# Kernel optimization log

Hardware: AMD Instinct MI355X
Metric: run time of the kernel (lower is better)

Reference implementation:

```python
import jax, jax.numpy as jnp
import numpy as np

N = 50000          # nodes
E = 1000000        # edges (avg degree 20)
F_IN = 16          # fluidFeatures
LAYERS = [64, 64, 64, 2]
TERMS = 4          # basisTerms
DIM = 2            # spatial dim
EDGE_DIM = TERMS * DIM  # mode='cat' -> terms * dim = 8
OUT_SCALE = 1.0 / 128.0  # outputScaling


def fourier_basis(n_terms, x):
    """Fourier basis ('ffourier'): k=0 -> 1, odd k -> sin(pi*ceil(k/2)*x), even k -> cos(pi*(k/2)*x). x: [E] -> [E, n_terms]."""
    cols = []
    for k in range(n_terms):
        if k == 0:
            cols.append(jnp.ones_like(x))
        elif k % 2 == 1:
            cols.append(jnp.sin(jnp.pi * ((k + 1) // 2) * x))
        else:
            cols.append(jnp.cos(jnp.pi * (k // 2) * x))
    return jnp.stack(cols, axis=-1)


def edge_basis(edge_lengths):
    # basisEncoderLayer with mode='cat': per-component basis, concatenated -> [E, TERMS*DIM]
    return jnp.concatenate([fourier_basis(TERMS, edge_lengths[:, d]) for d in range(DIM)], axis=1)


def setup_inputs() -> dict:
    key = jax.random.key(0)
    k_x, k_ei, k_el, k_w = jax.random.split(key, 4)
    x = jax.random.normal(k_x, (N, F_IN), dtype=jnp.float32)
    edge_index = jax.random.randint(k_ei, (2, E), 0, N)
    edge_lengths = jax.random.uniform(k_el, (E, DIM), dtype=jnp.float32, minval=-1.0, maxval=1.0)
    # continuous-conv weights: [EDGE_DIM, in_feat, out_feat] per layer (uniform-style init)
    weights = {}
    in_f = F_IN
    wkeys = jax.random.split(k_w, len(LAYERS))
    for i, out_f in enumerate(LAYERS):
        scale = 1.0 / np.sqrt(EDGE_DIM * in_f)
        weights[f"W{i}"] = scale * jax.random.normal(wkeys[i], (EDGE_DIM, in_f, out_f), dtype=jnp.float32)
        in_f = out_f
    return dict(x=x, edge_index=edge_index, edge_lengths=edge_lengths, **weights)


def reference(x, edge_index, edge_lengths, W0, W1, W2, W3):
    src = edge_index[0]
    dst = edge_index[1]
    basis = edge_basis(edge_lengths)            # [E, EDGE_DIM]
    Ws = [W0, W1, W2, W3]
    h = x
    for i, W in enumerate(Ws):
        # gather sender features, contract with per-edge basis and conv weight, scatter-sum to receivers
        msg = jnp.einsum('eb,ef,bfo->eo', basis, h[src], W)   # [E, out]
        agg = jax.ops.segment_sum(msg, dst, num_segments=N)   # [N, out]
        h = jax.nn.relu(agg) if i < len(Ws) - 1 else agg
    return h * OUT_SCALE
```

## Files before the change

kernel.cpp:

```cpp
#include <hip/hip_runtime.h>
#include <hip/hip_bf16.h>
#include <math.h>

#define PI_F 3.14159265358979323846f
#define BK_SHIFT 8
#define P2_CHUNK 4096
#define P2_PER_THREAD 16

typedef __attribute__((ext_vector_type(8))) short bf16x8;
typedef __attribute__((ext_vector_type(4))) float f32x4;
typedef __attribute__((ext_vector_type(4))) unsigned short u16x4;
typedef __attribute__((ext_vector_type(8))) unsigned short u16x8;

__device__ __forceinline__ float bf2f(unsigned short u) {
    union { unsigned int i; float f; } v;
    v.i = ((unsigned int)u) << 16;
    return v.f;
}

__device__ __forceinline__ unsigned short f2bf_bits(float f) {
    __hip_bfloat16 b = __float2bfloat16(f);
    unsigned short u;
    __builtin_memcpy(&u, &b, 2);
    return u;
}


__global__ void count_kernel(const int* __restrict__ dst, int* __restrict__ cnt, int E) {
    int e = blockIdx.x * 256 + threadIdx.x;
    if (e < E) atomicAdd(&cnt[dst[e]], 1);
}

__global__ __launch_bounds__(256) void scan_reduce_kernel(const int* __restrict__ cnt,
                                                          int* __restrict__ bsum, int n) {
    __shared__ int sd[4];
    int idx = blockIdx.x * 256 + threadIdx.x;
    int v = (idx < n) ? cnt[idx] : 0;
    int s = v;
#pragma unroll
    for (int m = 1; m < 64; m <<= 1) s += __shfl_xor(s, m, 64);
    int wave = threadIdx.x >> 6;
    if ((threadIdx.x & 63) == 0) sd[wave] = s;
    __syncthreads();
    if (threadIdx.x == 0) bsum[blockIdx.x] = sd[0] + sd[1] + sd[2] + sd[3];
}

__global__ __launch_bounds__(256) void scan_top_kernel(const int* __restrict__ bsum,
                                                       int* __restrict__ boffs, int nb) {
    __shared__ int sd[256];
    int tid = threadIdx.x;
    int v = (tid < nb) ? bsum[tid] : 0;
    sd[tid] = v;
    __syncthreads();
#pragma unroll
    for (int off = 1; off < 256; off <<= 1) {
        int t = (tid >= off) ? sd[tid - off] : 0;
        __syncthreads();
        sd[tid] += t;
        __syncthreads();
    }
    if (tid < nb) boffs[tid] = sd[tid] - v;
}

__global__ __launch_bounds__(256) void scan_apply_kernel(int* __restrict__ cntcur,
                                                         int* __restrict__ offs,
                                                         const int* __restrict__ boffs,
                                                         int n, int total) {
    __shared__ int sd[256];
    int tid = threadIdx.x;
    int idx = blockIdx.x * 256 + tid;
    int v = (idx < n) ? cntcur[idx] : 0;
    sd[tid] = v;
    __syncthreads();
#pragma unroll
    for (int off = 1; off < 256; off <<= 1) {
        int t = (tid >= off) ? sd[tid - off] : 0;
        __syncthreads();
        sd[tid] += t;
        __syncthreads();
    }
    if (idx < n) offs[idx] = boffs[blockIdx.x] + sd[tid] - v;
    if (idx == 0) offs[n] = total;
}

__global__ void bucket_init_kernel(const int* __restrict__ offs, int* __restrict__ bucketCursor,
                                   int nbuk, int nN) {
    int b = blockIdx.x * 256 + threadIdx.x;
    if (b < nbuk) bucketCursor[b] = offs[min(b << BK_SHIFT, nN)];
}

__global__ __launch_bounds__(256) void bucket_scatter_kernel(const int* __restrict__ dst,
                                                             int* __restrict__ bucketCursor,
                                                             int* __restrict__ inter,
                                                             int E, int nbuk) {
    __shared__ int lcnt[256];
    __shared__ int lbase[256];
    __shared__ int lgpos[256];
    __shared__ int lsort[P2_CHUNK];
    __shared__ unsigned char lbuk[P2_CHUNK];
    int tid = threadIdx.x;
    int base = blockIdx.x * P2_CHUNK;
    lcnt[tid] = 0;
    __syncthreads();
    int myb[P2_PER_THREAD], myr[P2_PER_THREAD];
#pragma unroll
    for (int i = 0; i < P2_PER_THREAD; i++) {
        int idx = base + i * 256 + tid;
        int b = -1, r = 0;
        if (idx < E) {
            b = dst[idx] >> BK_SHIFT;
            r = atomicAdd(&lcnt[b], 1);
        }
        myb[i] = b;
        myr[i] = r;
    }
    __syncthreads();
    int v = lcnt[tid];
    lbase[tid] = v;
    __syncthreads();
    for (int off = 1; off < 256; off <<= 1) {
        int t = (tid >= off) ? lbase[tid - off] : 0;
        __syncthreads();
        lbase[tid] += t;
        __syncthreads();
    }
    int excl = lbase[tid] - v;
    if (tid < nbuk && v > 0) lgpos[tid] = atomicAdd(&bucketCursor[tid], v);
    __syncthreads();
    lbase[tid] = excl;
    __syncthreads();
#pragma unroll
    for (int i = 0; i < P2_PER_THREAD; i++) {
        if (myb[i] >= 0) {
            int p = lbase[myb[i]] + myr[i];
            lsort[p] = base + i * 256 + tid;
            lbuk[p] = (unsigned char)myb[i];
        }
    }
    __syncthreads();
    int total = (base + P2_CHUNK <= E) ? P2_CHUNK : (E > base ? E - base : 0);
    for (int idx = tid; idx < total; idx += 256) {
        int b = lbuk[idx];
        inter[lgpos[b] + (idx - lbase[b])] = lsort[idx];
    }
}

__global__ __launch_bounds__(256) void bucket_sort_fill_kernel(const int* __restrict__ inter,
                                                               const int* __restrict__ dst,
                                                               const int* __restrict__ src,
                                                               const float* __restrict__ el,
                                                               const int* __restrict__ offs,
                                                               int* __restrict__ srcS,
                                                               unsigned short* __restrict__ basisB,
                                                               int nN) {
    __shared__ int cursor[256];
    int b = blockIdx.x;
    int n0 = b << BK_SHIFT;
    int n1 = min(n0 + 256, nN);
    int tid = threadIdx.x;
    int p0 = offs[n0];
    int p1 = offs[n1];
    if (tid < n1 - n0) cursor[tid] = offs[n0 + tid];
    __syncthreads();
    for (int q = p0 + tid; q < p1; q += 256) {
        int e = inter[q];
        int d = dst[e];
        int pos = atomicAdd(&cursor[d - n0], 1);
        srcS[pos] = src[e];
        float2 xy = *(const float2*)(el + 2 * (size_t)e);
        u16x8 p;
        p[0] = f2bf_bits(1.0f);
        p[1] = f2bf_bits(__sinf(PI_F * xy.x));
        p[2] = f2bf_bits(__cosf(PI_F * xy.x));
        p[3] = f2bf_bits(__sinf(2.0f * PI_F * xy.x));
        p[4] = f2bf_bits(1.0f);
        p[5] = f2bf_bits(__sinf(PI_F * xy.y));
        p[6] = f2bf_bits(__cosf(PI_F * xy.y));
        p[7] = f2bf_bits(__sinf(2.0f * PI_F * xy.y));
        *(u16x8*)(basisB + (size_t)pos * 8) = p;
    }
}


__global__ void prep_w_kernel(const float* __restrict__ W, __hip_bfloat16* __restrict__ Wt, int K) {
    int i = blockIdx.x * 256 + threadIdx.x;
    if (i >= K * 64) return;
    int k = i >> 6, o = i & 63;
    Wt[(size_t)o * K + k] = __float2bfloat16(W[i]);
}

__global__ void prep_f2b_kernel(const float* __restrict__ in, __hip_bfloat16* __restrict__ out, int n) {
    int i = blockIdx.x * 256 + threadIdx.x;
    if (i < n) out[i] = __float2bfloat16(in[i]);
}


__device__ __forceinline__ void agg64_core(const unsigned short* __restrict__ hp,
                                           const int* __restrict__ srcS,
                                           const unsigned short* __restrict__ basisB,
                                           int start, int end, int eg, int fb,
                                           float acc[8][4]) {
    const int last = end - 1;
    int j = start;
    int qa = min(j + eg, last), qb = min(j + 4 + eg, last);
    int sa = srcS[qa], sb = srcS[qb];
    u16x4 ga = *(const u16x4*)(hp + (size_t)sa * 64 + fb);
    u16x4 gb = *(const u16x4*)(hp + (size_t)sb * 64 + fb);
    u16x8 ca = *(const u16x8*)(basisB + (size_t)qa * 8);
    u16x8 cb = *(const u16x8*)(basisB + (size_t)qb * 8);
    int qna = min(j + 8 + eg, last), qnb = min(j + 12 + eg, last);
    int sna = srcS[qna], snb = srcS[qnb];
    while (true) {
        int jn = j + 8;
        int q2a = min(jn + 8 + eg, last), q2b = min(jn + 12 + eg, last);
        int s2a = srcS[q2a], s2b = srcS[q2b];
        u16x4 gna = *(const u16x4*)(hp + (size_t)sna * 64 + fb);
        u16x4 gnb = *(const u16x4*)(hp + (size_t)snb * 64 + fb);
        u16x8 cna = *(const u16x8*)(basisB + (size_t)qna * 8);
        u16x8 cnb = *(const u16x8*)(basisB + (size_t)qnb * 8);
        float ha[4], hb[4];
        ha[0] = bf2f(ga[0]); ha[1] = bf2f(ga[1]); ha[2] = bf2f(ga[2]); ha[3] = bf2f(ga[3]);
        hb[0] = bf2f(gb[0]); hb[1] = bf2f(gb[1]); hb[2] = bf2f(gb[2]); hb[3] = bf2f(gb[3]);
        if (j + eg >= end)     { ha[0] = 0.f; ha[1] = 0.f; ha[2] = 0.f; ha[3] = 0.f; }
        if (j + 4 + eg >= end) { hb[0] = 0.f; hb[1] = 0.f; hb[2] = 0.f; hb[3] = 0.f; }
#pragma unroll
        for (int b = 0; b < 8; b++) {
            float w = bf2f(ca[b]);
#pragma unroll
            for (int c = 0; c < 4; c++) acc[b][c] += w * ha[c];
        }
#pragma unroll
        for (int b = 0; b < 8; b++) {
            float w = bf2f(cb[b]);
#pragma unroll
            for (int c = 0; c < 4; c++) acc[b][c] += w * hb[c];
        }
        if (jn >= end) break;
        j = jn;
        ga = gna; gb = gnb; ca = cna; cb = cnb;
        qna = q2a; qnb = q2b; sna = s2a; snb = s2b;
    }
}

__global__ __launch_bounds__(256) void agg64_kernel(const __hip_bfloat16* __restrict__ h,
                                                    const int* __restrict__ srcS,
                                                    const unsigned short* __restrict__ basisB,
                                                    const int* __restrict__ offs,
                                                    __hip_bfloat16* __restrict__ A, int nN) {
    int wid = (blockIdx.x * 256 + threadIdx.x) >> 6;
    int lane = threadIdx.x & 63;
    if (wid >= nN) return;
    int eg = lane >> 4, fg = lane & 15;
    int start = offs[wid], end = offs[wid + 1];
    float acc[8][4] = {};
    if (start < end)
        agg64_core((const unsigned short*)h, srcS, basisB, start, end, eg, fg * 4, acc);
#pragma unroll
    for (int b = 0; b < 8; b++) {
#pragma unroll
        for (int c = 0; c < 4; c++) {
            float v = acc[b][c];
            v += __shfl_xor(v, 16, 64);
            v += __shfl_xor(v, 32, 64);
            acc[b][c] = v;
        }
    }
    if (eg == 0) {
        unsigned short* Ar = (unsigned short*)A + (size_t)wid * 512;
#pragma unroll
        for (int b = 0; b < 8; b++) {
            u16x4 p;
            p[0] = f2bf_bits(acc[b][0]); p[1] = f2bf_bits(acc[b][1]);
            p[2] = f2bf_bits(acc[b][2]); p[3] = f2bf_bits(acc[b][3]);
            *(u16x4*)(Ar + b * 64 + fg * 4) = p;
        }
    }
}

__global__ __launch_bounds__(256) void agg_out_kernel(const __hip_bfloat16* __restrict__ h,
                                                      const int* __restrict__ srcS,
                                                      const unsigned short* __restrict__ basisB,
                                                      const int* __restrict__ offs,
                                                      const float* __restrict__ W3,
                                                      float* __restrict__ out, int nN) {
    int wid = (blockIdx.x * 256 + threadIdx.x) >> 6;
    int lane = threadIdx.x & 63;
    if (wid >= nN) return;
    int eg = lane >> 4, fg = lane & 15;
    int start = offs[wid], end = offs[wid + 1];
    float acc[8][4] = {};
    if (start < end)
        agg64_core((const unsigned short*)h, srcS, basisB, start, end, eg, fg * 4, acc);
#pragma unroll
    for (int b = 0; b < 8; b++) {
#pragma unroll
        for (int c = 0; c < 4; c++) {
            float v = acc[b][c];
            v += __shfl_xor(v, 16, 64);
            v += __shfl_xor(v, 32, 64);
            acc[b][c] = v;
        }
    }
    float o0 = 0.f, o1 = 0.f;
#pragma unroll
    for (int b = 0; b < 8; b++) {
        const float* w = W3 + (size_t)(b * 64 + fg * 4) * 2;
        float4 wa = *(const float4*)w;
        float4 wb = *(const float4*)(w + 4);
        o0 += acc[b][0] * wa.x + acc[b][1] * wa.z + acc[b][2] * wb.x + acc[b][3] * wb.z;
        o1 += acc[b][0] * wa.y + acc[b][1] * wa.w + acc[b][2] * wb.y + acc[b][3] * wb.w;
    }
#pragma unroll
    for (int m = 1; m < 16; m <<= 1) {
        o0 += __shfl_xor(o0, m, 64);
        o1 += __shfl_xor(o1, m, 64);
    }
    if (lane == 0) {
        out[(size_t)wid * 2 + 0] = o0 * (1.0f / 128.0f);
        out[(size_t)wid * 2 + 1] = o1 * (1.0f / 128.0f);
    }
}


__global__ __launch_bounds__(256) void agg16_kernel(const __hip_bfloat16* __restrict__ h,
                                                    const int* __restrict__ srcS,
                                                    const unsigned short* __restrict__ basisB,
                                                    const int* __restrict__ offs,
                                                    __hip_bfloat16* __restrict__ A, int nN) {
    int wid = (blockIdx.x * 256 + threadIdx.x) >> 6;
    int lane = threadIdx.x & 63;
    if (wid >= nN) return;
    int eg = lane >> 2, fg = lane & 3;
    int start = offs[wid], end = offs[wid + 1];
    float acc[8][4] = {};
    if (start < end) {
        const unsigned short* hp = (const unsigned short*)h;
        const int last = end - 1;
        const int fb = fg * 4;
        int j = start;
        int q = min(j + eg, last);
        int s = srcS[q];
        u16x4 g = *(const u16x4*)(hp + (size_t)s * 16 + fb);
        u16x8 cbv = *(const u16x8*)(basisB + (size_t)q * 8);
        int qn = min(j + 16 + eg, last);
        int sn = srcS[qn];
        while (true) {
            int jn = j + 16;
            int q2 = min(jn + 16 + eg, last);
            int s2 = srcS[q2];
            u16x4 gn = *(const u16x4*)(hp + (size_t)sn * 16 + fb);
            u16x8 cn = *(const u16x8*)(basisB + (size_t)qn * 8);
            float hv[4];
            hv[0] = bf2f(g[0]); hv[1] = bf2f(g[1]); hv[2] = bf2f(g[2]); hv[3] = bf2f(g[3]);
            if (j + eg >= end) { hv[0] = 0.f; hv[1] = 0.f; hv[2] = 0.f; hv[3] = 0.f; }
#pragma unroll
            for (int b = 0; b < 8; b++) {
                float w = bf2f(cbv[b]);
#pragma unroll
                for (int c = 0; c < 4; c++) acc[b][c] += w * hv[c];
            }
            if (jn >= end) break;
            j = jn;
            g = gn; cbv = cn; qn = q2; sn = s2;
        }
    }
#pragma unroll
    for (int b = 0; b < 8; b++) {
#pragma unroll
        for (int c = 0; c < 4; c++) {
            float v = acc[b][c];
            v += __shfl_xor(v, 4, 64);
            v += __shfl_xor(v, 8, 64);
            v += __shfl_xor(v, 16, 64);
            v += __shfl_xor(v, 32, 64);
            acc[b][c] = v;
        }
    }
    if (eg == 0) {
        unsigned short* Ar = (unsigned short*)A + (size_t)wid * 128;
#pragma unroll
        for (int b = 0; b < 8; b++) {
            u16x4 p;
            p[0] = f2bf_bits(acc[b][0]); p[1] = f2bf_bits(acc[b][1]);
            p[2] = f2bf_bits(acc[b][2]); p[3] = f2bf_bits(acc[b][3]);
            *(u16x4*)(Ar + b * 16 + fg * 4) = p;
        }
    }
}


template <int K, bool RELU>
__global__ __launch_bounds__(256) void gemm_mfma_kernel(const __hip_bfloat16* __restrict__ A,
                                                        const __hip_bfloat16* __restrict__ Wt,
                                                        __hip_bfloat16* __restrict__ Hout, int nN) {
    int wave = threadIdx.x >> 6;
    int lane = threadIdx.x & 63;
    int m16 = lane & 15;
    int kg = lane >> 4;
    int arow = blockIdx.x * 64 + wave * 16 + m16;
    bool rowok = arow < nN;
    const short* Ap = (const short*)A;
    const short* Wp = (const short*)Wt;
    size_t abase = (size_t)arow * K + kg * 8;
    size_t wb0 = (size_t)(0 * 16 + m16) * K + kg * 8;
    size_t wb1 = (size_t)(1 * 16 + m16) * K + kg * 8;
    size_t wb2 = (size_t)(2 * 16 + m16) * K + kg * 8;
    size_t wb3 = (size_t)(3 * 16 + m16) * K + kg * 8;
    f32x4 acc0 = {0.f, 0.f, 0.f, 0.f};
    f32x4 acc1 = {0.f, 0.f, 0.f, 0.f};
    f32x4 acc2 = {0.f, 0.f, 0.f, 0.f};
    f32x4 acc3 = {0.f, 0.f, 0.f, 0.f};
#pragma unroll 4
    for (int kc = 0; kc < K; kc += 32) {
        bf16x8 af = {};
        if (rowok) af = *(const bf16x8*)(Ap + abase + kc);
        bf16x8 b0 = *(const bf16x8*)(Wp + wb0 + kc);
        bf16x8 b1 = *(const bf16x8*)(Wp + wb1 + kc);
        bf16x8 b2 = *(const bf16x8*)(Wp + wb2 + kc);
        bf16x8 b3 = *(const bf16x8*)(Wp + wb3 + kc);
        acc0 = __builtin_amdgcn_mfma_f32_16x16x32_bf16(af, b0, acc0, 0, 0, 0);
        acc1 = __builtin_amdgcn_mfma_f32_16x16x32_bf16(af, b1, acc1, 0, 0, 0);
        acc2 = __builtin_amdgcn_mfma_f32_16x16x32_bf16(af, b2, acc2, 0, 0, 0);
        acc3 = __builtin_amdgcn_mfma_f32_16x16x32_bf16(af, b3, acc3, 0, 0, 0);
    }
    int orow0 = blockIdx.x * 64 + wave * 16 + kg * 4;
#pragma unroll
    for (int r = 0; r < 4; r++) {
        int row = orow0 + r;
        if (row < nN) {
            float v0 = acc0[r], v1 = acc1[r], v2 = acc2[r], v3 = acc3[r];
            if (RELU) {
                v0 = fmaxf(v0, 0.0f); v1 = fmaxf(v1, 0.0f);
                v2 = fmaxf(v2, 0.0f); v3 = fmaxf(v3, 0.0f);
            }
            __hip_bfloat16* Hr = Hout + (size_t)row * 64;
            Hr[0 * 16 + m16] = __float2bfloat16(v0);
            Hr[1 * 16 + m16] = __float2bfloat16(v1);
            Hr[2 * 16 + m16] = __float2bfloat16(v2);
            Hr[3 * 16 + m16] = __float2bfloat16(v3);
        }
    }
}


extern "C" void kernel_launch(void* const* d_in, const int* in_sizes, int n_in,
                              void* d_out, int out_size, void* d_ws, size_t ws_size,
                              hipStream_t stream) {
    const float* x  = (const float*)d_in[0];
    const int*   ei = (const int*)d_in[1];
    const float* el = (const float*)d_in[2];
    const float* W0 = (const float*)d_in[3];
    const float* W1 = (const float*)d_in[4];
    const float* W2 = (const float*)d_in[5];
    const float* W3 = (const float*)d_in[6];
    int nN = in_sizes[0] / 16;
    int E  = in_sizes[1] / 2;
    const int* src = ei;
    const int* dst = ei + E;

    char* ws = (char*)d_ws;
    size_t off = 0;
    auto alloc = [&](size_t bytes) -> void* {
        void* p = ws + off;
        off = (off + bytes + 255) & ~(size_t)255;
        return p;
    };
    int nsb  = (nN + 255) / 256;
    int nbuk = (nN + 255) >> BK_SHIFT;
    int*   cntcur = (int*)alloc((size_t)(nN + 1) * 4);
    int*   offs   = (int*)alloc((size_t)(nN + 1) * 4);
    int*   bsum   = (int*)alloc((size_t)nsb * 4);
    int*   boffs  = (int*)alloc((size_t)nsb * 4);
    int*   bukcur = (int*)alloc((size_t)nbuk * 4);
    int*   inter  = (int*)alloc((size_t)E * 4);
    int*   srcS   = (int*)alloc((size_t)E * 4);
    unsigned short* basisB = (unsigned short*)alloc((size_t)E * 8 * 2);
    __hip_bfloat16* Ab  = (__hip_bfloat16*)alloc((size_t)nN * 512 * 2);
    __hip_bfloat16* Wt0 = (__hip_bfloat16*)alloc((size_t)64 * 128 * 2);
    __hip_bfloat16* Wt1 = (__hip_bfloat16*)alloc((size_t)64 * 512 * 2);
    __hip_bfloat16* Wt2 = (__hip_bfloat16*)alloc((size_t)64 * 512 * 2);
    __hip_bfloat16* xb  = (__hip_bfloat16*)alloc((size_t)nN * 16 * 2);
    __hip_bfloat16* hA  = (__hip_bfloat16*)alloc((size_t)nN * 64 * 2);
    __hip_bfloat16* hB  = (__hip_bfloat16*)alloc((size_t)nN * 64 * 2);
    (void)ws_size;

    hipMemsetAsync(cntcur, 0, (size_t)nN * 4, stream);
    int eb = (E + 255) / 256;
    count_kernel<<<eb, 256, 0, stream>>>(dst, cntcur, E);
    scan_reduce_kernel<<<nsb, 256, 0, stream>>>(cntcur, bsum, nN);
    scan_top_kernel<<<1, 256, 0, stream>>>(bsum, boffs, nsb);
    scan_apply_kernel<<<nsb, 256, 0, stream>>>(cntcur, offs, boffs, nN, E);
    bucket_init_kernel<<<(nbuk + 255) / 256, 256, 0, stream>>>(offs, bukcur, nbuk, nN);
    int p2b = (E + P2_CHUNK - 1) / P2_CHUNK;
    bucket_scatter_kernel<<<p2b, 256, 0, stream>>>(dst, bukcur, inter, E, nbuk);
    bucket_sort_fill_kernel<<<nbuk, 256, 0, stream>>>(inter, dst, src, el, offs, srcS, basisB, nN);

    prep_w_kernel<<<(128 * 64 + 255) / 256, 256, 0, stream>>>(W0, Wt0, 128);
    prep_w_kernel<<<(512 * 64 + 255) / 256, 256, 0, stream>>>(W1, Wt1, 512);
    prep_w_kernel<<<(512 * 64 + 255) / 256, 256, 0, stream>>>(W2, Wt2, 512);
    prep_f2b_kernel<<<(nN * 16 + 255) / 256, 256, 0, stream>>>(x, xb, nN * 16);

    int nb = (nN + 3) / 4;
    int gb = (nN + 63) / 64;

    agg16_kernel<<<nb, 256, 0, stream>>>(xb, srcS, basisB, offs, Ab, nN);
    gemm_mfma_kernel<128, true><<<gb, 256, 0, stream>>>(Ab, Wt0, hA, nN);
    agg64_kernel<<<nb, 256, 0, stream>>>(hA, srcS, basisB, offs, Ab, nN);
    gemm_mfma_kernel<512, true><<<gb, 256, 0, stream>>>(Ab, Wt1, hB, nN);
    agg64_kernel<<<nb, 256, 0, stream>>>(hB, srcS, basisB, offs, Ab, nN);
    gemm_mfma_kernel<512, true><<<gb, 256, 0, stream>>>(Ab, Wt2, hA, nN);
    agg_out_kernel<<<nb, 256, 0, stream>>>(hA, srcS, basisB, offs, W3, (float*)d_out, nN);
}
```

Before: 418.7 us.

## Process four nodes per wave in aggregation kernels with cross-node srcS prefetch

Each wave in the agg16, agg64 and output aggregation kernels now handles four consecutive destination nodes instead of one. It loads all segment boundaries up front and prefetches the first source indices of the next node while finishing the current one. This amortises per-wave launch and offset-load latency and hides the dependent srcS-then-gather latency chain at node boundaries. In exchange the grid has a quarter as many waves, which can lower occupancy and latency hiding and worsen load balance across uneven node degrees.

```diff
diff --git a/kernel.cpp b/kernel.cpp
--- a/kernel.cpp
+++ b/kernel.cpp
@@ -6,6 +6,7 @@
 #define BK_SHIFT 8
 #define P2_CHUNK 4096
 #define P2_PER_THREAD 16
+#define NPW 4
 
 typedef __attribute__((ext_vector_type(8))) short bf16x8;
 typedef __attribute__((ext_vector_type(4))) float f32x4;
@@ -195,21 +196,21 @@
 }
 
 
-__device__ __forceinline__ void agg64_core(const unsigned short* __restrict__ hp,
+__device__ __forceinline__ void agg64_body(const unsigned short* __restrict__ hp,
                                            const int* __restrict__ srcS,
                                            const unsigned short* __restrict__ basisB,
                                            int start, int end, int eg, int fb,
+                                           int sa, int sb,
                                            float acc[8][4]) {
     const int last = end - 1;
-    int j = start;
-    int qa = min(j + eg, last), qb = min(j + 4 + eg, last);
-    int sa = srcS[qa], sb = srcS[qb];
+    int qa = min(start + eg, last), qb = min(start + 4 + eg, last);
     u16x4 ga = *(const u16x4*)(hp + (size_t)sa * 64 + fb);
     u16x4 gb = *(const u16x4*)(hp + (size_t)sb * 64 + fb);
     u16x8 ca = *(const u16x8*)(basisB + (size_t)qa * 8);
     u16x8 cb = *(const u16x8*)(basisB + (size_t)qb * 8);
-    int qna = min(j + 8 + eg, last), qnb = min(j + 12 + eg, last);
+    int qna = min(start + 8 + eg, last), qnb = min(start + 12 + eg, last);
     int sna = srcS[qna], snb = srcS[qnb];
+    int j = start;
     while (true) {
         int jn = j + 8;
         int q2a = min(jn + 8 + eg, last), q2b = min(jn + 12 + eg, last);
@@ -249,30 +250,50 @@
                                                     __hip_bfloat16* __restrict__ A, int nN) {
     int wid = (blockIdx.x * 256 + threadIdx.x) >> 6;
     int lane = threadIdx.x & 63;
-    if (wid >= nN) return;
-    int eg = lane >> 4, fg = lane & 15;
-    int start = offs[wid], end = offs[wid + 1];
-    float acc[8][4] = {};
-    if (start < end)
-        agg64_core((const unsigned short*)h, srcS, basisB, start, end, eg, fg * 4, acc);
-#pragma unroll
-    for (int b = 0; b < 8; b++) {
-#pragma unroll
-        for (int c = 0; c < 4; c++) {
-            float v = acc[b][c];
-            v += __shfl_xor(v, 16, 64);
-            v += __shfl_xor(v, 32, 64);
-            acc[b][c] = v;
-        }
-    }
-    if (eg == 0) {
-        unsigned short* Ar = (unsigned short*)A + (size_t)wid * 512;
-#pragma unroll
-        for (int b = 0; b < 8; b++) {
-            u16x4 p;
-            p[0] = f2bf_bits(acc[b][0]); p[1] = f2bf_bits(acc[b][1]);
-            p[2] = f2bf_bits(acc[b][2]); p[3] = f2bf_bits(acc[b][3]);
-            *(u16x4*)(Ar + b * 64 + fg * 4) = p;
+    int nbase = wid * NPW;
+    if (nbase >= nN) return;
+    int eg = lane >> 4, fg = lane & 15, fb = fg * 4;
+    const unsigned short* hp = (const unsigned short*)h;
+    int bnd[NPW + 1];
+#pragma unroll
+    for (int i = 0; i <= NPW; i++) bnd[i] = offs[min(nbase + i, nN)];
+    int pa, pb;
+    {
+        int l0 = max(bnd[1] - 1, 0);
+        pa = srcS[min(bnd[0] + eg, l0)];
+        pb = srcS[min(bnd[0] + 4 + eg, l0)];
+    }
+#pragma unroll
+    for (int i = 0; i < NPW; i++) {
+        int n = nbase + i;
+        int start = bnd[i], end = bnd[i + 1];
+        float acc[8][4] = {};
+        if (start < end)
+            agg64_body(hp, srcS, basisB, start, end, eg, fb, pa, pb, acc);
+        if (i < NPW - 1) {
+            int l1 = max(bnd[i + 2] - 1, 0);
+            pa = srcS[min(bnd[i + 1] + eg, l1)];
+            pb = srcS[min(bnd[i + 1] + 4 + eg, l1)];
+        }
+#pragma unroll
+        for (int b = 0; b < 8; b++) {
+#pragma unroll
+            for (int c = 0; c < 4; c++) {
+                float v = acc[b][c];
+                v += __shfl_xor(v, 16, 64);
+                v += __shfl_xor(v, 32, 64);
+                acc[b][c] = v;
+            }
+        }
+        if (eg == 0 && n < nN) {
+            unsigned short* Ar = (unsigned short*)A + (size_t)n * 512;
+#pragma unroll
+            for (int b = 0; b < 8; b++) {
+                u16x4 p;
+                p[0] = f2bf_bits(acc[b][0]); p[1] = f2bf_bits(acc[b][1]);
+                p[2] = f2bf_bits(acc[b][2]); p[3] = f2bf_bits(acc[b][3]);
+                *(u16x4*)(Ar + b * 64 + fb) = p;
+            }
         }
     }
 }
@@ -285,42 +306,96 @@
                                                       float* __restrict__ out, int nN) {
     int wid = (blockIdx.x * 256 + threadIdx.x) >> 6;
     int lane = threadIdx.x & 63;
-    if (wid >= nN) return;
-    int eg = lane >> 4, fg = lane & 15;
-    int start = offs[wid], end = offs[wid + 1];
-    float acc[8][4] = {};
-    if (start < end)
-        agg64_core((const unsigned short*)h, srcS, basisB, start, end, eg, fg * 4, acc);
-#pragma unroll
-    for (int b = 0; b < 8; b++) {
-#pragma unroll
-        for (int c = 0; c < 4; c++) {
-            float v = acc[b][c];
-            v += __shfl_xor(v, 16, 64);
-            v += __shfl_xor(v, 32, 64);
-            acc[b][c] = v;
-        }
-    }
-    float o0 = 0.f, o1 = 0.f;
-#pragma unroll
-    for (int b = 0; b < 8; b++) {
-        const float* w = W3 + (size_t)(b * 64 + fg * 4) * 2;
-        float4 wa = *(const float4*)w;
-        float4 wb = *(const float4*)(w + 4);
-        o0 += acc[b][0] * wa.x + acc[b][1] * wa.z + acc[b][2] * wb.x + acc[b][3] * wb.z;
-        o1 += acc[b][0] * wa.y + acc[b][1] * wa.w + acc[b][2] * wb.y + acc[b][3] * wb.w;
-    }
-#pragma unroll
-    for (int m = 1; m < 16; m <<= 1) {
-        o0 += __shfl_xor(o0, m, 64);
-        o1 += __shfl_xor(o1, m, 64);
-    }
-    if (lane == 0) {
-        out[(size_t)wid * 2 + 0] = o0 * (1.0f / 128.0f);
-        out[(size_t)wid * 2 + 1] = o1 * (1.0f / 128.0f);
-    }
-}
-
+    int nbase = wid * NPW;
+    if (nbase >= nN) return;
+    int eg = lane >> 4, fg = lane & 15, fb = fg * 4;
+    const unsigned short* hp = (const unsigned short*)h;
+    int bnd[NPW + 1];
+#pragma unroll
+    for (int i = 0; i <= NPW; i++) bnd[i] = offs[min(nbase + i, nN)];
+    int pa, pb;
+    {
+        int l0 = max(bnd[1] - 1, 0);
+        pa = srcS[min(bnd[0] + eg, l0)];
+        pb = srcS[min(bnd[0] + 4 + eg, l0)];
+    }
+#pragma unroll
+    for (int i = 0; i < NPW; i++) {
+        int n = nbase + i;
+        int start = bnd[i], end = bnd[i + 1];
+        float acc[8][4] = {};
+        if (start < end)
+            agg64_body(hp, srcS, basisB, start, end, eg, fb, pa, pb, acc);
+        if (i < NPW - 1) {
+            int l1 = max(bnd[i + 2] - 1, 0);
+            pa = srcS[min(bnd[i + 1] + eg, l1)];
+            pb = srcS[min(bnd[i + 1] + 4 + eg, l1)];
+        }
+#pragma unroll
+        for (int b = 0; b < 8; b++) {
+#pragma unroll
+            for (int c = 0; c < 4; c++) {
+                float v = acc[b][c];
+                v += __shfl_xor(v, 16, 64);
+                v += __shfl_xor(v, 32, 64);
+                acc[b][c] = v;
+            }
+        }
+        float o0 = 0.f, o1 = 0.f;
+#pragma unroll
+        for (int b = 0; b < 8; b++) {
+            const float* w = W3 + (size_t)(b * 64 + fb) * 2;
+            float4 wa = *(const float4*)w;
+            float4 wb = *(const float4*)(w + 4);
+            o0 += acc[b][0] * wa.x + acc[b][1] * wa.z + acc[b][2] * wb.x + acc[b][3] * wb.z;
+            o1 += acc[b][0] * wa.y + acc[b][1] * wa.w + acc[b][2] * wb.y + acc[b][3] * wb.w;
+        }
+#pragma unroll
+        for (int m = 1; m < 16; m <<= 1) {
+            o0 += __shfl_xor(o0, m, 64);
+            o1 += __shfl_xor(o1, m, 64);
+        }
+        if (lane == 0 && n < nN) {
+            out[(size_t)n * 2 + 0] = o0 * (1.0f / 128.0f);
+            out[(size_t)n * 2 + 1] = o1 * (1.0f / 128.0f);
+        }
+    }
+}
+
+
+__device__ __forceinline__ void agg16_body(const unsigned short* __restrict__ hp,
+                                           const int* __restrict__ srcS,
+                                           const unsigned short* __restrict__ basisB,
+                                           int start, int end, int eg, int fb,
+                                           int s0,
+                                           float acc[8][4]) {
+    const int last = end - 1;
+    int q = min(start + eg, last);
+    u16x4 g = *(const u16x4*)(hp + (size_t)s0 * 16 + fb);
+    u16x8 cbv = *(const u16x8*)(basisB + (size_t)q * 8);
+    int qn = min(start + 16 + eg, last);
+    int sn = srcS[qn];
+    int j = start;
+    while (true) {
+        int jn = j + 16;
+        int q2 = min(jn + 16 + eg, last);
+        int s2 = srcS[q2];
+        u16x4 gn = *(const u16x4*)(hp + (size_t)sn * 16 + fb);
+        u16x8 cn = *(const u16x8*)(basisB + (size_t)qn * 8);
+        float hv[4];
+        hv[0] = bf2f(g[0]); hv[1] = bf2f(g[1]); hv[2] = bf2f(g[2]); hv[3] = bf2f(g[3]);
+        if (j + eg >= end) { hv[0] = 0.f; hv[1] = 0.f; hv[2] = 0.f; hv[3] = 0.f; }
+#pragma unroll
+        for (int b = 0; b < 8; b++) {
+            float w = bf2f(cbv[b]);
+#pragma unroll
+            for (int c = 0; c < 4; c++) acc[b][c] += w * hv[c];
+        }
+        if (jn >= end) break;
+        j = jn;
+        g = gn; cbv = cn; qn = q2; sn = s2;
+    }
+}
 
 __global__ __launch_bounds__(256) void agg16_kernel(const __hip_bfloat16* __restrict__ h,
                                                     const int* __restrict__ srcS,
@@ -329,61 +404,50 @@
                                                     __hip_bfloat16* __restrict__ A, int nN) {
     int wid = (blockIdx.x * 256 + threadIdx.x) >> 6;
     int lane = threadIdx.x & 63;
-    if (wid >= nN) return;
-    int eg = lane >> 2, fg = lane & 3;
-    int start = offs[wid], end = offs[wid + 1];
-    float acc[8][4] = {};
-    if (start < end) {
-        const unsigned short* hp = (const unsigned short*)h;
-        const int last = end - 1;
-        const int fb = fg * 4;
-        int j = start;
-        int q = min(j + eg, last);
-        int s = srcS[q];
-        u16x4 g = *(const u16x4*)(hp + (size_t)s * 16 + fb);
-        u16x8 cbv = *(const u16x8*)(basisB + (size_t)q * 8);
-        int qn = min(j + 16 + eg, last);
-        int sn = srcS[qn];
-        while (true) {
-            int jn = j + 16;
-            int q2 = min(jn + 16 + eg, last);
-            int s2 = srcS[q2];
-            u16x4 gn = *(const u16x4*)(hp + (size_t)sn * 16 + fb);
-            u16x8 cn = *(const u16x8*)(basisB + (size_t)qn * 8);
-            float hv[4];
-            hv[0] = bf2f(g[0]); hv[1] = bf2f(g[1]); hv[2] = bf2f(g[2]); hv[3] = bf2f(g[3]);
-            if (j + eg >= end) { hv[0] = 0.f; hv[1] = 0.f; hv[2] = 0.f; hv[3] = 0.f; }
+    int nbase = wid * NPW;
+    if (nbase >= nN) return;
+    int eg = lane >> 2, fg = lane & 3, fb = fg * 4;
+    const unsigned short* hp = (const unsigned short*)h;
+    int bnd[NPW + 1];
+#pragma unroll
+    for (int i = 0; i <= NPW; i++) bnd[i] = offs[min(nbase + i, nN)];
+    int pa;
+    {
+        int l0 = max(bnd[1] - 1, 0);
+        pa = srcS[min(bnd[0] + eg, l0)];
+    }
+#pragma unroll
+    for (int i = 0; i < NPW; i++) {
+        int n = nbase + i;
+        int start = bnd[i], end = bnd[i + 1];
+        float acc[8][4] = {};
+        if (start < end)
+            agg16_body(hp, srcS, basisB, start, end, eg, fb, pa, acc);
+        if (i < NPW - 1) {
+            int l1 = max(bnd[i + 2] - 1, 0);
+            pa = srcS[min(bnd[i + 1] + eg, l1)];
+        }
+#pragma unroll
+        for (int b = 0; b < 8; b++) {
+#pragma unroll
+            for (int c = 0; c < 4; c++) {
+                float v = acc[b][c];
+                v += __shfl_xor(v, 4, 64);
+                v += __shfl_xor(v, 8, 64);
+                v += __shfl_xor(v, 16, 64);
+                v += __shfl_xor(v, 32, 64);
+                acc[b][c] = v;
+            }
+        }
+        if (eg == 0 && n < nN) {
+            unsigned short* Ar = (unsigned short*)A + (size_t)n * 128;
 #pragma unroll
             for (int b = 0; b < 8; b++) {
-                float w = bf2f(cbv[b]);
-#pragma unroll
-                for (int c = 0; c < 4; c++) acc[b][c] += w * hv[c];
+                u16x4 p;
+                p[0] = f2bf_bits(acc[b][0]); p[1] = f2bf_bits(acc[b][1]);
+                p[2] = f2bf_bits(acc[b][2]); p[3] = f2bf_bits(acc[b][3]);
+                *(u16x4*)(Ar + b * 16 + fb) = p;
             }
-            if (jn >= end) break;
-            j = jn;
-            g = gn; cbv = cn; qn = q2; sn = s2;
-        }
-    }
-#pragma unroll
-    for (int b = 0; b < 8; b++) {
-#pragma unroll
-        for (int c = 0; c < 4; c++) {
-            float v = acc[b][c];
-            v += __shfl_xor(v, 4, 64);
-            v += __shfl_xor(v, 8, 64);
-            v += __shfl_xor(v, 16, 64);
-            v += __shfl_xor(v, 32, 64);
-            acc[b][c] = v;
-        }
-    }
-    if (eg == 0) {
-        unsigned short* Ar = (unsigned short*)A + (size_t)wid * 128;
-#pragma unroll
-        for (int b = 0; b < 8; b++) {
-            u16x4 p;
-            p[0] = f2bf_bits(acc[b][0]); p[1] = f2bf_bits(acc[b][1]);
-            p[2] = f2bf_bits(acc[b][2]); p[3] = f2bf_bits(acc[b][3]);
-            *(u16x4*)(Ar + b * 16 + fg * 4) = p;
         }
     }
 }
@@ -500,7 +564,8 @@
     prep_w_kernel<<<(512 * 64 + 255) / 256, 256, 0, stream>>>(W2, Wt2, 512);
     prep_f2b_kernel<<<(nN * 16 + 255) / 256, 256, 0, stream>>>(x, xb, nN * 16);
 
-    int nb = (nN + 3) / 4;
+    int waves = (nN + NPW - 1) / NPW;
+    int nb = (waves + 3) / 4;
     int gb = (nN + 63) / 64;
 
     agg16_kernel<<<nb, 256, 0, stream>>>(xb, srcS, basisB, offs, Ab, nN);
```

Result: slower. 457.0 us (+9.2%).

## Replace per-node count and scan with bucket-level histogram and in-block node offsets

Applied to the files above, without the earlier changes.

Drops the global per-node atomic count and the three-kernel scan over node counts. A per-chunk bucket histogram in shared memory with one global scan feeds the scatter, and each bucket block then builds its own per-node histogram and prefix scan to produce CSR offsets. Bucket edge ids and local destinations are cached in shared memory up to a fixed capacity so the fill pass avoids re-reading them from global memory. This removes one million global atomics and several kernel launches. In exchange the sort-fill kernel does extra work and uses more shared memory, which may lower its occupancy.

```diff
diff --git a/kernel.cpp b/kernel.cpp
--- a/kernel.cpp
+++ b/kernel.cpp
@@ -6,6 +6,7 @@
 #define BK_SHIFT 8
 #define P2_CHUNK 4096
 #define P2_PER_THREAD 16
+#define BCAP 6144
 
 typedef __attribute__((ext_vector_type(8))) short bf16x8;
 typedef __attribute__((ext_vector_type(4))) float f32x4;
@@ -26,30 +27,28 @@
 }
 
 
-__global__ void count_kernel(const int* __restrict__ dst, int* __restrict__ cnt, int E) {
-    int e = blockIdx.x * 256 + threadIdx.x;
-    if (e < E) atomicAdd(&cnt[dst[e]], 1);
-}
-
-__global__ __launch_bounds__(256) void scan_reduce_kernel(const int* __restrict__ cnt,
-                                                          int* __restrict__ bsum, int n) {
-    __shared__ int sd[4];
-    int idx = blockIdx.x * 256 + threadIdx.x;
-    int v = (idx < n) ? cnt[idx] : 0;
-    int s = v;
-#pragma unroll
-    for (int m = 1; m < 64; m <<= 1) s += __shfl_xor(s, m, 64);
-    int wave = threadIdx.x >> 6;
-    if ((threadIdx.x & 63) == 0) sd[wave] = s;
-    __syncthreads();
-    if (threadIdx.x == 0) bsum[blockIdx.x] = sd[0] + sd[1] + sd[2] + sd[3];
-}
-
-__global__ __launch_bounds__(256) void scan_top_kernel(const int* __restrict__ bsum,
-                                                       int* __restrict__ boffs, int nb) {
+__global__ __launch_bounds__(256) void bucket_count_kernel(const int* __restrict__ dst,
+                                                           int* __restrict__ bcnt, int E, int nbuk) {
+    __shared__ int h[256];
+    int tid = threadIdx.x;
+    h[tid] = 0;
+    __syncthreads();
+    int base = blockIdx.x * P2_CHUNK;
+    for (int i = tid; i < P2_CHUNK; i += 256) {
+        int idx = base + i;
+        if (idx < E) atomicAdd(&h[dst[idx] >> BK_SHIFT], 1);
+    }
+    __syncthreads();
+    if (tid < nbuk && h[tid] > 0) atomicAdd(&bcnt[tid], h[tid]);
+}
+
+__global__ __launch_bounds__(256) void bucket_scan_kernel(const int* __restrict__ bcnt,
+                                                          int* __restrict__ bukbase,
+                                                          int* __restrict__ bukcur,
+                                                          int nbuk, int E) {
     __shared__ int sd[256];
     int tid = threadIdx.x;
-    int v = (tid < nb) ? bsum[tid] : 0;
+    int v = (tid < nbuk) ? bcnt[tid] : 0;
     sd[tid] = v;
     __syncthreads();
 #pragma unroll
@@ -59,34 +58,12 @@
         sd[tid] += t;
         __syncthreads();
     }
-    if (tid < nb) boffs[tid] = sd[tid] - v;
-}
-
-__global__ __launch_bounds__(256) void scan_apply_kernel(int* __restrict__ cntcur,
-                                                         int* __restrict__ offs,
-                                                         const int* __restrict__ boffs,
-                                                         int n, int total) {
-    __shared__ int sd[256];
-    int tid = threadIdx.x;
-    int idx = blockIdx.x * 256 + tid;
-    int v = (idx < n) ? cntcur[idx] : 0;
-    sd[tid] = v;
-    __syncthreads();
-#pragma unroll
-    for (int off = 1; off < 256; off <<= 1) {
-        int t = (tid >= off) ? sd[tid - off] : 0;
-        __syncthreads();
-        sd[tid] += t;
-        __syncthreads();
-    }
-    if (idx < n) offs[idx] = boffs[blockIdx.x] + sd[tid] - v;
-    if (idx == 0) offs[n] = total;
-}
-
-__global__ void bucket_init_kernel(const int* __restrict__ offs, int* __restrict__ bucketCursor,
-                                   int nbuk, int nN) {
-    int b = blockIdx.x * 256 + threadIdx.x;
-    if (b < nbuk) bucketCursor[b] = offs[min(b << BK_SHIFT, nN)];
+    if (tid < nbuk) {
+        int ex = sd[tid] - v;
+        bukbase[tid] = ex;
+        bukcur[tid] = ex;
+    }
+    if (tid == 0) bukbase[nbuk] = E;
 }
 
 __global__ __launch_bounds__(256) void bucket_scatter_kernel(const int* __restrict__ dst,
@@ -149,23 +126,53 @@
                                                                const int* __restrict__ dst,
                                                                const int* __restrict__ src,
                                                                const float* __restrict__ el,
-                                                               const int* __restrict__ offs,
+                                                               const int* __restrict__ bukbase,
+                                                               int* __restrict__ offs,
                                                                int* __restrict__ srcS,
                                                                unsigned short* __restrict__ basisB,
-                                                               int nN) {
+                                                               int nN, int nbuk) {
+    __shared__ int hist[256];
     __shared__ int cursor[256];
+    __shared__ int eloc[BCAP];
+    __shared__ unsigned char dloc[BCAP];
     int b = blockIdx.x;
     int n0 = b << BK_SHIFT;
     int n1 = min(n0 + 256, nN);
+    int nn = n1 - n0;
     int tid = threadIdx.x;
-    int p0 = offs[n0];
-    int p1 = offs[n1];
-    if (tid < n1 - n0) cursor[tid] = offs[n0 + tid];
-    __syncthreads();
-    for (int q = p0 + tid; q < p1; q += 256) {
-        int e = inter[q];
-        int d = dst[e];
-        int pos = atomicAdd(&cursor[d - n0], 1);
+    int p0 = bukbase[b], p1 = bukbase[b + 1];
+    int cnt = p1 - p0;
+    bool cached = (cnt <= BCAP);
+    hist[tid] = 0;
+    __syncthreads();
+    for (int i = tid; i < cnt; i += 256) {
+        int e = inter[p0 + i];
+        int d = dst[e] - n0;
+        if (cached) { eloc[i] = e; dloc[i] = (unsigned char)d; }
+        atomicAdd(&hist[d], 1);
+    }
+    __syncthreads();
+    int v = hist[tid];
+    cursor[tid] = v;
+    __syncthreads();
+#pragma unroll
+    for (int off = 1; off < 256; off <<= 1) {
+        int t = (tid >= off) ? cursor[tid - off] : 0;
+        __syncthreads();
+        cursor[tid] += t;
+        __syncthreads();
+    }
+    int ex = cursor[tid] - v;
+    if (tid < nn) offs[n0 + tid] = p0 + ex;
+    if (b == nbuk - 1 && tid == 0) offs[nN] = p1;
+    __syncthreads();
+    cursor[tid] = p0 + ex;
+    __syncthreads();
+    for (int i = tid; i < cnt; i += 256) {
+        int e, d;
+        if (cached) { e = eloc[i]; d = dloc[i]; }
+        else        { e = inter[p0 + i]; d = dst[e] - n0; }
+        int pos = atomicAdd(&cursor[d], 1);
         srcS[pos] = src[e];
         float2 xy = *(const float2*)(el + 2 * (size_t)e);
         u16x8 p;
@@ -465,15 +472,13 @@
         off = (off + bytes + 255) & ~(size_t)255;
         return p;
     };
-    int nsb  = (nN + 255) / 256;
     int nbuk = (nN + 255) >> BK_SHIFT;
-    int*   cntcur = (int*)alloc((size_t)(nN + 1) * 4);
-    int*   offs   = (int*)alloc((size_t)(nN + 1) * 4);
-    int*   bsum   = (int*)alloc((size_t)nsb * 4);
-    int*   boffs  = (int*)alloc((size_t)nsb * 4);
-    int*   bukcur = (int*)alloc((size_t)nbuk * 4);
-    int*   inter  = (int*)alloc((size_t)E * 4);
-    int*   srcS   = (int*)alloc((size_t)E * 4);
+    int*   bcnt    = (int*)alloc((size_t)nbuk * 4);
+    int*   bukbase = (int*)alloc((size_t)(nbuk + 1) * 4);
+    int*   bukcur  = (int*)alloc((size_t)nbuk * 4);
+    int*   offs    = (int*)alloc((size_t)(nN + 1) * 4);
+    int*   inter   = (int*)alloc((size_t)E * 4);
+    int*   srcS    = (int*)alloc((size_t)E * 4);
     unsigned short* basisB = (unsigned short*)alloc((size_t)E * 8 * 2);
     __hip_bfloat16* Ab  = (__hip_bfloat16*)alloc((size_t)nN * 512 * 2);
     __hip_bfloat16* Wt0 = (__hip_bfloat16*)alloc((size_t)64 * 128 * 2);
@@ -484,16 +489,13 @@
     __hip_bfloat16* hB  = (__hip_bfloat16*)alloc((size_t)nN * 64 * 2);
     (void)ws_size;
 
-    hipMemsetAsync(cntcur, 0, (size_t)nN * 4, stream);
-    int eb = (E + 255) / 256;
-    count_kernel<<<eb, 256, 0, stream>>>(dst, cntcur, E);
-    scan_reduce_kernel<<<nsb, 256, 0, stream>>>(cntcur, bsum, nN);
-    scan_top_kernel<<<1, 256, 0, stream>>>(bsum, boffs, nsb);
-    scan_apply_kernel<<<nsb, 256, 0, stream>>>(cntcur, offs, boffs, nN, E);
-    bucket_init_kernel<<<(nbuk + 255) / 256, 256, 0, stream>>>(offs, bukcur, nbuk, nN);
+    hipMemsetAsync(bcnt, 0, (size_t)nbuk * 4, stream);
     int p2b = (E + P2_CHUNK - 1) / P2_CHUNK;
+    bucket_count_kernel<<<p2b, 256, 0, stream>>>(dst, bcnt, E, nbuk);
+    bucket_scan_kernel<<<1, 256, 0, stream>>>(bcnt, bukbase, bukcur, nbuk, E);
     bucket_scatter_kernel<<<p2b, 256, 0, stream>>>(dst, bukcur, inter, E, nbuk);
-    bucket_sort_fill_kernel<<<nbuk, 256, 0, stream>>>(inter, dst, src, el, offs, srcS, basisB, nN);
+    bucket_sort_fill_kernel<<<nbuk, 256, 0, stream>>>(inter, dst, src, el, bukbase, offs,
+                                                      srcS, basisB, nN, nbuk);
 
     prep_w_kernel<<<(128 * 64 + 255) / 256, 256, 0, stream>>>(W0, Wt0, 128);
     prep_w_kernel<<<(512 * 64 + 255) / 256, 256, 0, stream>>>(W1, Wt1, 512);
```

Result: faster. 383.0 us, median of 2 (-8.5%).
